# Optimization experiments

Hardware: AMD Instinct MI355X
Metric: run time of the kernel (lower is better)

The kernel has to match this reference:

```python
import jax, jax.numpy as jnp
import numpy as np

N, D, IN_DIM, H, L = 20000, 32, 3, 64, 3


def _lstm_agg(h_nodes, nbr_sorted, W_ih, W_hh, b_ih, b_hh):
    """Batched LSTM over each node's (sorted) neighbor sequence; returns final hidden state h_T."""
    n = h_nodes.shape[0]
    hidden = W_hh.shape[1]

    def step(carry, idx):
        h, c = carry
        x = h_nodes[idx]                                     # [N, in_d] irregular gather
        gates = x @ W_ih.T + h @ W_hh.T + b_ih + b_hh        # [N, 4H], torch gate order i,f,g,o
        i_g, f_g, g_g, o_g = jnp.split(gates, 4, axis=-1)
        c = jax.nn.sigmoid(f_g) * c + jax.nn.sigmoid(i_g) * jnp.tanh(g_g)
        h = jax.nn.sigmoid(o_g) * jnp.tanh(c)
        return (h, c), None

    init = (jnp.zeros((n, hidden), h_nodes.dtype), jnp.zeros((n, hidden), h_nodes.dtype))
    (h_T, _), _ = jax.lax.scan(step, init, nbr_sorted.T)      # scan over D neighbor slots
    return h_T


def _layer(h, nbr_sorted, W_ih, W_hh, b_ih, b_hh, Wl, bl):
    agg = _lstm_agg(h, nbr_sorted, W_ih, W_hh, b_ih, b_hh)    # [N, H]
    comb = jnp.concatenate([h, agg], axis=-1)                 # [N, in_d + H]
    return jax.nn.relu(comb @ Wl.T + bl)


def _forward(node_features, nbr, params, W_out, b_out):
    nbr_sorted = jnp.sort(nbr, axis=1)   # permutation-invariant ordering (Eq. 9)
    h = node_features
    for p in params:
        h = _layer(h, nbr_sorted, *p)
    return (h @ W_out.T + b_out).squeeze(-1)   # [N] per-node log-likelihood scores


def setup_inputs():
    key = jax.random.key(0)
    ks = jax.random.split(key, 40)
    inp = {}
    inp["node_features"] = jax.random.normal(ks[0], (N, IN_DIM), jnp.float32)
    inp["nbr"] = jax.random.randint(ks[1], (N, D), 0, N, jnp.int32)
    k = 2
    s = 1.0 / np.sqrt(H)
    for l in range(L):
        in_d = IN_DIM if l == 0 else H
        inp[f"W_ih{l}"] = (jax.random.normal(ks[k], (4 * H, in_d)) * (1.0 / np.sqrt(in_d))).astype(jnp.float32); k += 1
        inp[f"W_hh{l}"] = (jax.random.normal(ks[k], (4 * H, H)) * s).astype(jnp.float32); k += 1
        inp[f"b_ih{l}"] = (jax.random.normal(ks[k], (4 * H,)) * s).astype(jnp.float32); k += 1
        inp[f"b_hh{l}"] = (jax.random.normal(ks[k], (4 * H,)) * s).astype(jnp.float32); k += 1
        inp[f"Wl{l}"] = (jax.random.normal(ks[k], (H, in_d + H)) * (1.0 / np.sqrt(in_d + H))).astype(jnp.float32); k += 1
        inp[f"bl{l}"] = (jax.random.normal(ks[k], (H,)) * s).astype(jnp.float32); k += 1
    inp["W_out"] = (jax.random.normal(ks[k], (1, H)) * s).astype(jnp.float32); k += 1
    inp["b_out"] = jnp.zeros((1,), jnp.float32)
    return inp


def reference(node_features, nbr, W_ih0, W_hh0, b_ih0, b_hh0, Wl0, bl0, W_ih1, W_hh1, b_ih1, b_hh1, Wl1, bl1, W_ih2, W_hh2, b_ih2, b_hh2, Wl2, bl2, W_out, b_out):
    params = [
        (W_ih0, W_hh0, b_ih0, b_hh0, Wl0, bl0),
        (W_ih1, W_hh1, b_ih1, b_hh1, Wl1, bl1),
        (W_ih2, W_hh2, b_ih2, b_hh2, Wl2, bl2),
    ]
    return _forward(node_features, nbr, params, W_out, b_out)
```

## Files before the change

kernel.cpp:

```cpp
#include <hip/hip_runtime.h>
#include <hip/hip_bf16.h>

#define NN 20000
#define NG 1250
#define LOG2E 1.44269504088896f
#define TWOLOG2E 2.88539008177793f
#define SORT_BLOCKS 79
#define PREP_BLOCKS 1024

typedef __attribute__((ext_vector_type(8))) short short8;
typedef __attribute__((ext_vector_type(4))) float floatx4;

__device__ __forceinline__ floatx4 MF(short8 a, short8 b, floatx4 c) {
    return __builtin_amdgcn_mfma_f32_16x16x32_bf16(a, b, c, 0, 0, 0);
}
__device__ __forceinline__ float ex2(float x) { return __builtin_amdgcn_exp2f(x); }
__device__ __forceinline__ float rcp(float x) { return __builtin_amdgcn_rcpf(x); }
__device__ __forceinline__ unsigned short bf16r(float x) {
    return __builtin_bit_cast(unsigned short, __float2bfloat16(x));
}
__device__ __forceinline__ void lds_barrier() {
    asm volatile("s_waitcnt lgkmcnt(0)\n\ts_barrier" ::: "memory");
}
__device__ __forceinline__ int rowswz(int L) {
    return L ^ (((L >> 4) & 1) << 1) ^ ((L >> 3) & 1);
}

#define PREP_TOT (49152 + 49152 + 12288 + 12288 + 768 + 640000)
__global__ void prep_sort_kernel(const float* __restrict__ x,
    const int* __restrict__ nbr, int* __restrict__ nbrT,
    const float* __restrict__ Wih0, const float* __restrict__ Whh0,
    const float* __restrict__ bih0, const float* __restrict__ bhh0, const float* __restrict__ Wl0,
    const float* __restrict__ Wih1, const float* __restrict__ Whh1,
    const float* __restrict__ bih1, const float* __restrict__ bhh1, const float* __restrict__ Wl1,
    const float* __restrict__ Wih2, const float* __restrict__ Whh2,
    const float* __restrict__ bih2, const float* __restrict__ bhh2, const float* __restrict__ Wl2,
    unsigned short* __restrict__ Wih_p, unsigned short* __restrict__ Whh_p,
    unsigned short* __restrict__ Wlx_p, unsigned short* __restrict__ Wlh_p,
    float* __restrict__ bsum, unsigned short* __restrict__ x32)
{
    if (blockIdx.x < SORT_BLOCKS) {
        int n = blockIdx.x * 256 + threadIdx.x;
        if (n >= NN) return;
        int v[32];
        const int4* src = (const int4*)(nbr + n * 32);
        #pragma unroll
        for (int i = 0; i < 8; i++) {
            int4 t = src[i];
            v[4*i] = t.x; v[4*i+1] = t.y; v[4*i+2] = t.z; v[4*i+3] = t.w;
        }
        #pragma unroll
        for (int k = 2; k <= 32; k <<= 1)
            #pragma unroll
            for (int j = k >> 1; j > 0; j >>= 1)
                #pragma unroll
                for (int i = 0; i < 32; i++) {
                    int ixj = i ^ j;
                    if (ixj > i) {
                        bool up = (i & k) == 0;
                        int a = v[i], b = v[ixj];
                        bool sw = up ? (a > b) : (a < b);
                        if (sw) { v[i] = b; v[ixj] = a; }
                    }
                }
        int g = n >> 4, m = n & 15;
        int base = g * 512 + m;
        #pragma unroll
        for (int t = 0; t < 32; t++) nbrT[base + t * 16] = v[t];
        return;
    }

    for (int i = (blockIdx.x - SORT_BLOCKS) * 256 + threadIdx.x; i < PREP_TOT;
         i += PREP_BLOCKS * 256) {
        int j = i;
        if (j < 49152) {
            int l = j >> 14, e = j & 16383;
            if (l == 0) {
                if (e < 8192) {
                    int col = e >> 5, k = e & 31;
                    float sc = (col >= 128 && col < 192) ? TWOLOG2E : LOG2E;
                    float v = (k < 3) ? Wih0[col*3 + k] * sc : 0.f;
                    Wih_p[e] = bf16r(v);
                }
            } else {
                int col = e >> 6, k = e & 63;
                const float* W = (l == 1) ? Wih1 : Wih2;
                float sc = (col >= 128 && col < 192) ? TWOLOG2E : LOG2E;
                Wih_p[l*16384 + e] = bf16r(W[col*64 + k] * sc);
            }
            continue;
        }
        j -= 49152;
        if (j < 49152) {
            int l = j >> 14, e = j & 16383;
            int col = e >> 6, k = e & 63;
            const float* W = (l == 0) ? Whh0 : ((l == 1) ? Whh1 : Whh2);
            float sc = (col >= 128 && col < 192) ? TWOLOG2E : LOG2E;
            Whh_p[l*16384 + e] = bf16r(W[col*64 + k] * sc);
            continue;
        }
        j -= 49152;
        if (j < 12288) {
            int l = j >> 12, e = j & 4095;
            if (l == 0) {
                if (e < 2048) {
                    int col = e >> 5, k = e & 31;
                    float v = (k < 3) ? Wl0[col*67 + k] : 0.f;
                    Wlx_p[e] = bf16r(v);
                }
            } else {
                int col = e >> 6, k = e & 63;
                const float* W = (l == 1) ? Wl1 : Wl2;
                Wlx_p[l*4096 + e] = bf16r(W[col*128 + k]);
            }
            continue;
        }
        j -= 12288;
        if (j < 12288) {
            int l = j >> 12, e = j & 4095;
            int col = e >> 6, k = e & 63;
            float v = (l == 0) ? Wl0[col*67 + 3 + k]
                               : ((l == 1) ? Wl1 : Wl2)[col*128 + 64 + k];
            Wlh_p[l*4096 + e] = bf16r(v);
            continue;
        }
        j -= 12288;
        if (j < 768) {
            int l = j >> 8, col = j & 255;
            const float* bi = (l == 0) ? bih0 : ((l == 1) ? bih1 : bih2);
            const float* bh = (l == 0) ? bhh0 : ((l == 1) ? bhh1 : bhh2);
            float sc = (col >= 128 && col < 192) ? TWOLOG2E : LOG2E;
            bsum[l*256 + col] = (bi[col] + bh[col]) * sc;
            continue;
        }
        j -= 768;
        {
            int n = j >> 5, k = j & 31;
            x32[j] = bf16r((k < 3) ? x[n*3 + k] : 0.f);
        }
    }
}

template<int XKC, int LASTL>
__global__ __launch_bounds__(256, 4)
void lstm_mfma_kernel(const unsigned short* __restrict__ xsrc,
                      const int* __restrict__ nbrT,
                      const unsigned short* __restrict__ Wih,
                      const unsigned short* __restrict__ Whh,
                      const float* __restrict__ bsum,
                      const unsigned short* __restrict__ Wlx,
                      const unsigned short* __restrict__ Wlh,
                      const float* __restrict__ bl,
                      const float* __restrict__ W_out,
                      const float* __restrict__ b_out,
                      void* __restrict__ hout)
{
    __shared__ unsigned short sA[2][1024];
    __shared__ float sRed[64];

    const int w    = threadIdx.x >> 6;
    const int lane = threadIdx.x & 63;
    const int q    = lane >> 4;
    const int c    = lane & 15;
    const int XS   = XKC * 32;

    const int g = blockIdx.x;
    const int node0 = g * 16;
    const int* nbg = nbrT + g * 512;

    short8 fWih[4][XKC];
    short8 fWhh[4][2];
    float  biasv[4];
    #pragma unroll
    for (int t4 = 0; t4 < 4; t4++) {
        int col = 64*t4 + 16*w + c;
        biasv[t4] = bsum[col];
        #pragma unroll
        for (int kc = 0; kc < XKC; kc++)
            fWih[t4][kc] = *(const short8*)(Wih + col*XS + kc*32 + q*8);
        #pragma unroll
        for (int kc = 0; kc < 2; kc++)
            fWhh[t4][kc] = *(const short8*)(Whh + col*64 + kc*32 + q*8);
    }

    float cst[4] = {0.f, 0.f, 0.f, 0.f};
    short8 hA[2] = {};

    int idx_cur = nbg[c];
    int idx_nxt = nbg[16 + c];
    short8 xg[XKC];
    #pragma unroll
    for (int kc = 0; kc < XKC; kc++)
        xg[kc] = *(const short8*)(xsrc + (long)idx_cur * XS + kc*32 + q*8);

    const int u = 16*w + c;

    #pragma unroll 1
    for (int t = 0; t < 32; t++) {
        floatx4 acc[4];
        #pragma unroll
        for (int t4 = 0; t4 < 4; t4++) {
            floatx4 a; a[0] = biasv[t4]; a[1] = biasv[t4]; a[2] = biasv[t4]; a[3] = biasv[t4];
            acc[t4] = a;
        }
        if (t > 0) {
            #pragma unroll
            for (int t4 = 0; t4 < 4; t4++) {
                acc[t4] = MF(hA[0], fWhh[t4][0], acc[t4]);
                acc[t4] = MF(hA[1], fWhh[t4][1], acc[t4]);
            }
        }
        #pragma unroll
        for (int t4 = 0; t4 < 4; t4++)
            #pragma unroll
            for (int kc = 0; kc < XKC; kc++)
                acc[t4] = MF(xg[kc], fWih[t4][kc], acc[t4]);

        if (t < 31) {
            #pragma unroll
            for (int kc = 0; kc < XKC; kc++)
                xg[kc] = *(const short8*)(xsrc + (long)idx_nxt * XS + kc*32 + q*8);
            int tn = (t + 2 < 32) ? t + 2 : 31;
            idx_nxt = nbg[tn*16 + c];
        }

        unsigned short* sAb = sA[t & 1];
        #pragma unroll
        for (int r = 0; r < 4; r++) {
            float gi = acc[0][r], gf = acc[1][r], gg = acc[2][r], go = acc[3][r];
            float ei = ex2(-gi);
            float ef = ex2(-gf);
            float eo = ex2(-go);
            float eg = ex2(-__builtin_fabsf(gg));
            float P  = (1.f + ei) * (1.f + eg);
            float R  = rcp(P * (1.f + ef));
            float iG = __builtin_copysignf(1.f - eg, gg) * ((1.f + ef) * R);
            float cm = fmaf(cst[r], P * R, iG);
            cst[r] = cm;
            float ec = ex2(-TWOLOG2E * __builtin_fabsf(cm));
            float h  = __builtin_copysignf(1.f - ec, cm) * rcp((1.f + eo) * (1.f + ec));
            int row = (4*q + r) + 16*(u >> 3);
            sAb[rowswz(row)*8 + (u & 7)] = bf16r(h);
        }
        lds_barrier();
        hA[0] = *(const short8*)(sA[t & 1] + rowswz(lane)*8);
        hA[1] = *(const short8*)(sA[t & 1] + 512 + rowswz(lane)*8);
    }

    const int col = u;
    short8 fx[XKC], fh[2];
    float blv = bl[col];
    #pragma unroll
    for (int kc = 0; kc < XKC; kc++)
        fx[kc] = *(const short8*)(Wlx + col*XS + kc*32 + q*8);
    fh[0] = *(const short8*)(Wlh + col*64 + q*8);
    fh[1] = *(const short8*)(Wlh + col*64 + 32 + q*8);
    short8 hin[XKC];
    #pragma unroll
    for (int kc = 0; kc < XKC; kc++)
        hin[kc] = *(const short8*)(xsrc + (long)(node0 + c) * XS + kc*32 + q*8);

    floatx4 a; a[0] = blv; a[1] = blv; a[2] = blv; a[3] = blv;
    #pragma unroll
    for (int kc = 0; kc < XKC; kc++) a = MF(hin[kc], fx[kc], a);
    a = MF(hA[0], fh[0], a);
    a = MF(hA[1], fh[1], a);

    if (!LASTL) {
        #pragma unroll
        for (int r = 0; r < 4; r++)
            ((unsigned short*)hout)[(node0 + 4*q + r) * 64 + col] = bf16r(fmaxf(a[r], 0.f));
    } else {
        float wo = W_out[col];
        float p[4];
        #pragma unroll
        for (int r = 0; r < 4; r++) p[r] = fmaxf(a[r], 0.f) * wo;
        #pragma unroll
        for (int d = 1; d < 16; d <<= 1) {
            #pragma unroll
            for (int r = 0; r < 4; r++) p[r] += __shfl_xor(p[r], d);
        }
        if (c == 0) {
            #pragma unroll
            for (int r = 0; r < 4; r++) sRed[w*16 + 4*q + r] = p[r];
        }
        lds_barrier();
        if (w == 0 && lane < 16)
            ((float*)hout)[node0 + lane] =
                sRed[lane] + sRed[16 + lane] + sRed[32 + lane] + sRed[48 + lane] + b_out[0];
    }
}

extern "C" void kernel_launch(void* const* d_in, const int* in_sizes, int n_in,
                              void* d_out, int out_size, void* d_ws, size_t ws_size,
                              hipStream_t stream) {
    (void)in_sizes; (void)n_in; (void)out_size; (void)ws_size;
    const float* node_features = (const float*)d_in[0];
    const int*   nbr           = (const int*)d_in[1];
    const float* Wih[3] = {(const float*)d_in[2],  (const float*)d_in[8],  (const float*)d_in[14]};
    const float* Whh[3] = {(const float*)d_in[3],  (const float*)d_in[9],  (const float*)d_in[15]};
    const float* bih[3] = {(const float*)d_in[4],  (const float*)d_in[10], (const float*)d_in[16]};
    const float* bhh[3] = {(const float*)d_in[5],  (const float*)d_in[11], (const float*)d_in[17]};
    const float* Wl[3]  = {(const float*)d_in[6],  (const float*)d_in[12], (const float*)d_in[18]};
    const float* bl[3]  = {(const float*)d_in[7],  (const float*)d_in[13], (const float*)d_in[19]};
    const float* W_out  = (const float*)d_in[20];
    const float* b_out  = (const float*)d_in[21];

    char* ws = (char*)d_ws;
    int*            nbrT  = (int*)ws;
    unsigned short* x32   = (unsigned short*)(ws + 2560000);
    unsigned short* hb1   = (unsigned short*)(ws + 3840000);
    unsigned short* hb2   = (unsigned short*)(ws + 6400000);
    unsigned short* Wih_p = (unsigned short*)(ws + 8960000);
    unsigned short* Whh_p = (unsigned short*)(ws + 9058304);
    unsigned short* Wlx_p = (unsigned short*)(ws + 9156608);
    unsigned short* Wlh_p = (unsigned short*)(ws + 9181184);
    float*          bsum  = (float*)(ws + 9205760);

    prep_sort_kernel<<<SORT_BLOCKS + PREP_BLOCKS, 256, 0, stream>>>(node_features,
        nbr, nbrT,
        Wih[0], Whh[0], bih[0], bhh[0], Wl[0],
        Wih[1], Whh[1], bih[1], bhh[1], Wl[1],
        Wih[2], Whh[2], bih[2], bhh[2], Wl[2],
        Wih_p, Whh_p, Wlx_p, Wlh_p, bsum, x32);

    lstm_mfma_kernel<1, 0><<<NG, 256, 0, stream>>>(x32, nbrT,
        Wih_p,         Whh_p,         bsum,       Wlx_p,        Wlh_p,        bl[0],
        nullptr, nullptr, hb1);
    lstm_mfma_kernel<2, 0><<<NG, 256, 0, stream>>>(hb1, nbrT,
        Wih_p + 16384, Whh_p + 16384, bsum + 256, Wlx_p + 4096, Wlh_p + 4096, bl[1],
        nullptr, nullptr, hb2);
    lstm_mfma_kernel<2, 1><<<NG, 256, 0, stream>>>(hb2, nbrT,
        Wih_p + 32768, Whh_p + 32768, bsum + 512, Wlx_p + 8192, Wlh_p + 8192, bl[2],
        W_out, b_out, (float*)d_out);
}
```

Before: 324.7 us.

## Precompute input-gate projections per node and gather them in the LSTM loop

Adds a separate GEMM kernel that computes x·W_ih^T + bias once per node into a float workspace G. The recurrent kernel then gathers precomputed gate rows for each neighbor instead of gathering features and running the input MFMAs at every step, which drops 32x redundant input-projection work. It also raises the launch-bounds occupancy hint, since the W_ih fragments no longer occupy registers. The cost is three extra launches and a heavier gather: each neighbor now brings 1 KB of fp32 gates instead of 64–128 B of bf16 features.

```diff
diff --git a/kernel.cpp b/kernel.cpp
--- a/kernel.cpp
+++ b/kernel.cpp
@@ -141,13 +141,45 @@
     }
 }
 
+template<int XKC>
+__global__ __launch_bounds__(256, 4)
+void ggemm_kernel(const unsigned short* __restrict__ xsrc,
+                  const unsigned short* __restrict__ Wih,
+                  const float* __restrict__ bsum,
+                  float* __restrict__ G)
+{
+    const int w = threadIdx.x >> 6, lane = threadIdx.x & 63;
+    const int q = lane >> 4, c = lane & 15;
+    const int XS = XKC * 32;
+    const int node0 = blockIdx.x * 16;
+
+    short8 xa[XKC];
+    #pragma unroll
+    for (int kc = 0; kc < XKC; kc++)
+        xa[kc] = *(const short8*)(xsrc + (long)(node0 + c) * XS + kc*32 + q*8);
+
+    #pragma unroll
+    for (int t4 = 0; t4 < 4; t4++) {
+        int col = 64*t4 + 16*w + c;
+        float bv = bsum[col];
+        floatx4 a; a[0] = bv; a[1] = bv; a[2] = bv; a[3] = bv;
+        #pragma unroll
+        for (int kc = 0; kc < XKC; kc++) {
+            short8 fb = *(const short8*)(Wih + col*XS + kc*32 + q*8);
+            a = MF(xa[kc], fb, a);
+        }
+        #pragma unroll
+        for (int r = 0; r < 4; r++)
+            G[(long)(node0 + 4*q + r) * 256 + (16*w + c)*4 + t4] = a[r];
+    }
+}
+
 template<int XKC, int LASTL>
-__global__ __launch_bounds__(256, 4)
+__global__ __launch_bounds__(256, 5)
 void lstm_mfma_kernel(const unsigned short* __restrict__ xsrc,
                       const int* __restrict__ nbrT,
-                      const unsigned short* __restrict__ Wih,
+                      const float* __restrict__ G,
                       const unsigned short* __restrict__ Whh,
-                      const float* __restrict__ bsum,
                       const unsigned short* __restrict__ Wlx,
                       const unsigned short* __restrict__ Wlh,
                       const float* __restrict__ bl,
@@ -167,17 +199,12 @@
     const int g = blockIdx.x;
     const int node0 = g * 16;
     const int* nbg = nbrT + g * 512;
-
-    short8 fWih[4][XKC];
+    const int u = 16*w + c;
+
     short8 fWhh[4][2];
-    float  biasv[4];
     #pragma unroll
     for (int t4 = 0; t4 < 4; t4++) {
-        int col = 64*t4 + 16*w + c;
-        biasv[t4] = bsum[col];
-        #pragma unroll
-        for (int kc = 0; kc < XKC; kc++)
-            fWih[t4][kc] = *(const short8*)(Wih + col*XS + kc*32 + q*8);
+        int col = 64*t4 + u;
         #pragma unroll
         for (int kc = 0; kc < 2; kc++)
             fWhh[t4][kc] = *(const short8*)(Whh + col*64 + kc*32 + q*8);
@@ -186,21 +213,20 @@
     float cst[4] = {0.f, 0.f, 0.f, 0.f};
     short8 hA[2] = {};
 
-    int idx_cur = nbg[c];
-    int idx_nxt = nbg[16 + c];
-    short8 xg[XKC];
-    #pragma unroll
-    for (int kc = 0; kc < XKC; kc++)
-        xg[kc] = *(const short8*)(xsrc + (long)idx_cur * XS + kc*32 + q*8);
-
-    const int u = 16*w + c;
+    const long uoff = (long)u * 4;
+    int4 i4 = *(const int4*)(nbg + 4*q);
+    int4 i4n = *(const int4*)(nbg + 16 + 4*q);
+    floatx4 gr0 = *(const floatx4*)(G + (long)i4.x * 256 + uoff);
+    floatx4 gr1 = *(const floatx4*)(G + (long)i4.y * 256 + uoff);
+    floatx4 gr2 = *(const floatx4*)(G + (long)i4.z * 256 + uoff);
+    floatx4 gr3 = *(const floatx4*)(G + (long)i4.w * 256 + uoff);
 
     #pragma unroll 1
     for (int t = 0; t < 32; t++) {
         floatx4 acc[4];
         #pragma unroll
         for (int t4 = 0; t4 < 4; t4++) {
-            floatx4 a; a[0] = biasv[t4]; a[1] = biasv[t4]; a[2] = biasv[t4]; a[3] = biasv[t4];
+            floatx4 a; a[0] = gr0[t4]; a[1] = gr1[t4]; a[2] = gr2[t4]; a[3] = gr3[t4];
             acc[t4] = a;
         }
         if (t > 0) {
@@ -210,18 +236,14 @@
                 acc[t4] = MF(hA[1], fWhh[t4][1], acc[t4]);
             }
         }
-        #pragma unroll
-        for (int t4 = 0; t4 < 4; t4++)
-            #pragma unroll
-            for (int kc = 0; kc < XKC; kc++)
-                acc[t4] = MF(xg[kc], fWih[t4][kc], acc[t4]);
 
         if (t < 31) {
-            #pragma unroll
-            for (int kc = 0; kc < XKC; kc++)
-                xg[kc] = *(const short8*)(xsrc + (long)idx_nxt * XS + kc*32 + q*8);
+            gr0 = *(const floatx4*)(G + (long)i4n.x * 256 + uoff);
+            gr1 = *(const floatx4*)(G + (long)i4n.y * 256 + uoff);
+            gr2 = *(const floatx4*)(G + (long)i4n.z * 256 + uoff);
+            gr3 = *(const floatx4*)(G + (long)i4n.w * 256 + uoff);
             int tn = (t + 2 < 32) ? t + 2 : 31;
-            idx_nxt = nbg[tn*16 + c];
+            i4n = *(const int4*)(nbg + tn*16 + 4*q);
         }
 
         unsigned short* sAb = sA[t & 1];
@@ -316,6 +338,7 @@
     unsigned short* Wlx_p = (unsigned short*)(ws + 9156608);
     unsigned short* Wlh_p = (unsigned short*)(ws + 9181184);
     float*          bsum  = (float*)(ws + 9205760);
+    float*          G     = (float*)(ws + 9208832);
 
     prep_sort_kernel<<<SORT_BLOCKS + PREP_BLOCKS, 256, 0, stream>>>(node_features,
         nbr, nbrT,
@@ -324,13 +347,15 @@
         Wih[2], Whh[2], bih[2], bhh[2], Wl[2],
         Wih_p, Whh_p, Wlx_p, Wlh_p, bsum, x32);
 
-    lstm_mfma_kernel<1, 0><<<NG, 256, 0, stream>>>(x32, nbrT,
-        Wih_p,         Whh_p,         bsum,       Wlx_p,        Wlh_p,        bl[0],
-        nullptr, nullptr, hb1);
-    lstm_mfma_kernel<2, 0><<<NG, 256, 0, stream>>>(hb1, nbrT,
-        Wih_p + 16384, Whh_p + 16384, bsum + 256, Wlx_p + 4096, Wlh_p + 4096, bl[1],
-        nullptr, nullptr, hb2);
-    lstm_mfma_kernel<2, 1><<<NG, 256, 0, stream>>>(hb2, nbrT,
-        Wih_p + 32768, Whh_p + 32768, bsum + 512, Wlx_p + 8192, Wlh_p + 8192, bl[2],
-        W_out, b_out, (float*)d_out);
-}
+    ggemm_kernel<1><<<NG, 256, 0, stream>>>(x32, Wih_p, bsum, G);
+    lstm_mfma_kernel<1, 0><<<NG, 256, 0, stream>>>(x32, nbrT, G,
+        Whh_p,         Wlx_p,        Wlh_p,        bl[0], nullptr, nullptr, hb1);
+
+    ggemm_kernel<2><<<NG, 256, 0, stream>>>(hb1, Wih_p + 16384, bsum + 256, G);
+    lstm_mfma_kernel<2, 0><<<NG, 256, 0, stream>>>(hb1, nbrT, G,
+        Whh_p + 16384, Wlx_p + 4096, Wlh_p + 4096, bl[1], nullptr, nullptr, hb2);
+
+    ggemm_kernel<2><<<NG, 256, 0, stream>>>(hb2, Wih_p + 32768, bsum + 512, G);
+    lstm_mfma_kernel<2, 1><<<NG, 256, 0, stream>>>(hb2, nbrT, G,
+        Whh_p + 32768, Wlx_p + 8192, Wlh_p + 8192, bl[2], W_out, b_out, (float*)d_out);
+}
```

Result: slower. 406.4 us (+25.2%).
